# Kernel optimization log

Measured on AMD Instinct MI355X. Metric: run time of the kernel, lower is better.

Reference implementation:

```python
import jax, jax.numpy as jnp
import numpy as np

N = 50000
E = 800000
IN_C, HID_C, OUT_C = 512, 128, 64


def setup_inputs() -> dict:
    key = jax.random.key(0)
    k = jax.random.split(key, 8)
    x = jax.random.normal(k[0], (N, IN_C), dtype=jnp.float32)
    edge_index = jax.random.randint(k[1], (2, E), 0, N, dtype=jnp.int64)
    edge_weight = jax.random.uniform(k[2], (E,), dtype=jnp.float32)
    # GCNConv parameters (glorot-like init)
    W1 = jax.random.normal(k[3], (IN_C, HID_C), dtype=jnp.float32) * (1.0 / np.sqrt(IN_C))
    b1 = jnp.zeros((HID_C,), dtype=jnp.float32)
    W2 = jax.random.normal(k[4], (HID_C, OUT_C), dtype=jnp.float32) * (1.0 / np.sqrt(HID_C))
    b2 = jnp.zeros((OUT_C,), dtype=jnp.float32)
    return {"x": x, "edge_index": edge_index, "edge_weight": edge_weight,
            "W1": W1, "b1": b1, "W2": W2, "b2": b2}


def _add_self_loops(edge_index, edge_weight, num_nodes):
    loop = jnp.arange(num_nodes, dtype=edge_index.dtype)
    ei = jnp.concatenate([edge_index, jnp.stack([loop, loop])], axis=1)
    ew = jnp.concatenate([edge_weight, jnp.ones((num_nodes,), edge_weight.dtype)])
    return ei, ew


def _gcn_conv(x, row, col, norm, W, b, num_nodes):
    # linear transform first (PyG GCNConv), then normalized scatter-add aggregation
    xw = x @ W                                    # [N, F_out]
    msg = norm[:, None] * xw[row]                 # gather + scale, [E', F_out]
    out = jnp.zeros((num_nodes, xw.shape[1]), xw.dtype).at[col].add(msg)
    return out + b


def reference(x, edge_index, edge_weight, W1, b1, W2, b2):
    num_nodes = x.shape[0]
    ei, ew = _add_self_loops(edge_index, edge_weight, num_nodes)
    row, col = ei[0], ei[1]
    # symmetric normalization: D^{-1/2} A D^{-1/2} (deg over destination index)
    deg = jnp.zeros((num_nodes,), ew.dtype).at[col].add(ew)
    dinv = jnp.where(deg > 0, jax.lax.rsqrt(deg), 0.0)
    norm = dinv[row] * ew * dinv[col]
    h = _gcn_conv(x, row, col, norm, W1, b1, num_nodes)
    h = jax.nn.relu(h)
    # dropout p=0.5 is identity in eval mode
    return _gcn_conv(h, row, col, norm, W2, b2, num_nodes)
```

## Files before the change

### kernel.cpp

```cpp
#include <hip/hip_runtime.h>

#define NNODES 50000
#define NEDGES 800000
#define IN_C   512
#define HID_C  128
#define OUT_C  64
#define NBUCK  196
#define BCAP   5120
#define BREG   5376

typedef float  f32x4  __attribute__((ext_vector_type(4)));
typedef __bf16 bf16x8 __attribute__((ext_vector_type(8)));
typedef short  short8 __attribute__((ext_vector_type(8)));

#define GLDS(src, dst) \
  __builtin_amdgcn_global_load_lds( \
      (const __attribute__((address_space(1))) unsigned int*)(src), \
      (__attribute__((address_space(3))) unsigned int*)(dst), 16, 0, 0)

__device__ __forceinline__ float bf2f(unsigned short u) {
  unsigned int x = (unsigned int)u << 16;
  return __builtin_bit_cast(float, x);
}
__device__ __forceinline__ unsigned short f16bits(float f) {
  _Float16 h = (_Float16)f;
  return __builtin_bit_cast(unsigned short, h);
}
__device__ __forceinline__ float f16val(unsigned short u) {
  return (float)__builtin_bit_cast(_Float16, u);
}


__device__ __forceinline__ void wsplit_one(const float* __restrict__ W,
                                           unsigned short* __restrict__ Th,
                                           unsigned short* __restrict__ Tl,
                                           int K, int N, int id) {
  int k = id % K, n = id / K;
  float f = W[(size_t)k * N + n];
  __bf16 hb = (__bf16)f;
  __bf16 lb = (__bf16)(f - (float)hb);
  Th[id] = __builtin_bit_cast(unsigned short, hb);
  Tl[id] = __builtin_bit_cast(unsigned short, lb);
}

__global__ void __launch_bounds__(256) prep0_kernel(
    unsigned int* __restrict__ gclaim,
    const float* __restrict__ W1, unsigned short* __restrict__ W1th,
    unsigned short* __restrict__ W1tl,
    const float* __restrict__ W2, unsigned short* __restrict__ W2th,
    unsigned short* __restrict__ W2tl) {
  int id = blockIdx.x * blockDim.x + threadIdx.x;
  if (id < 256) { if (id < NBUCK) gclaim[id] = (unsigned int)id * BCAP; return; }
  int s = id - 256;
  if (s < IN_C * HID_C) wsplit_one(W1, W1th, W1tl, IN_C, HID_C, s);
  else if (s < IN_C * HID_C + HID_C * OUT_C)
    wsplit_one(W2, W2th, W2tl, HID_C, OUT_C, s - IN_C * HID_C);
}


__global__ void __launch_bounds__(1024) bin_scatter_kernel(
    const int* __restrict__ ei, const float* __restrict__ ew,
    unsigned int* __restrict__ gclaim, unsigned long long* __restrict__ binned, int nE) {
  __shared__ unsigned int h[NBUCK];
  __shared__ unsigned int cur[NBUCK];
  int t = threadIdx.x;
  if (t < NBUCK) h[t] = 0;
  __syncthreads();
  int base = blockIdx.x * 8192;
  int r[8]; unsigned int c[8]; unsigned short wb[8];
#pragma unroll
  for (int i = 0; i < 8; ++i) {
    int e = base + i * 1024 + t;
    if (e < nE) {
      r[i] = ei[e];
      c[i] = (unsigned int)ei[nE + e];
      wb[i] = f16bits(ew[e]);
      atomicAdd(&h[c[i] >> 8], 1u);
    } else {
      c[i] = 0xFFFFFFFFu;
    }
  }
  __syncthreads();
  if (t < NBUCK) cur[t] = h[t] ? atomicAdd(&gclaim[t], h[t]) : 0u;
  __syncthreads();
#pragma unroll
  for (int i = 0; i < 8; ++i) {
    if (c[i] != 0xFFFFFFFFu) {
      unsigned int pos = atomicAdd(&cur[c[i] >> 8], 1u);
      unsigned long long rec = (unsigned long long)((unsigned int)r[i] & 0xFFFFu)
                             | ((unsigned long long)(c[i] & 0xFFu) << 16)
                             | ((unsigned long long)wb[i] << 32);
      binned[pos] = rec;
    }
  }
}


__global__ void __launch_bounds__(256) bucket_deg_kernel(
    const unsigned long long* __restrict__ binned, const unsigned int* __restrict__ gclaim,
    float* __restrict__ dinv, int* __restrict__ offs, unsigned short* __restrict__ cnts) {
  int b = blockIdx.x, t = threadIdx.x;
  int base = b * BCAP;
  int cnt = (int)gclaim[b] - base;
  int nb = min(256, NNODES - b * 256);
  __shared__ unsigned int ec[256], wf[256];
  __shared__ int sc[256];
  ec[t] = 0; wf[t] = 0;
  __syncthreads();
  for (int i = t; i < cnt; i += 256) {
    unsigned long long rec = binned[base + i];
    int dlo = (int)((rec >> 16) & 255ULL);
    atomicAdd(&ec[dlo], 1u);
    float w = f16val((unsigned short)(rec >> 32));
    atomicAdd(&wf[dlo], (unsigned int)(w * 1048576.0f + 0.5f));
  }
  __syncthreads();
  int cn = (t < nb) ? (int)ec[t] + 1 : 0;
  sc[t] = cn;
  __syncthreads();
  for (int off = 1; off < 256; off <<= 1) {
    int u = (t >= off) ? sc[t - off] : 0;
    __syncthreads();
    sc[t] += u;
    __syncthreads();
  }
  if (t < nb) {
    float deg = (float)wf[t] * (1.0f / 1048576.0f) + 1.0f;
    int g = b * 256 + t;
    dinv[g] = rsqrtf(deg);
    offs[g] = b * BREG + sc[t] - cn;
    cnts[g] = (unsigned short)ec[t];
  }
}


__global__ void __launch_bounds__(256) bucket_fill_kernel(
    const unsigned long long* __restrict__ binned, const unsigned int* __restrict__ gclaim,
    const float* __restrict__ dinv, const int* __restrict__ offs,
    unsigned int* __restrict__ edges) {
  int b = blockIdx.x, t = threadIdx.x;
  int base = b * BCAP;
  int cnt = (int)gclaim[b] - base;
  int nb = min(256, NNODES - b * 256);
  int csrbase = b * BREG;
  __shared__ unsigned int image[BREG];
  __shared__ unsigned int cur[256];
  __shared__ float ldv[256];
  float di = 0.f;
  if (t < nb) {
    int g = b * 256 + t;
    di = dinv[g];
    int loc = offs[g] - csrbase;
    cur[t] = (unsigned int)(loc + 1);
    image[loc] = (unsigned int)g | ((unsigned int)f16bits(di * di) << 16);
  }
  ldv[t] = di;
  __syncthreads();
  for (int i = t; i < cnt; i += 256) {
    unsigned long long rec = binned[base + i];
    int src = (int)(rec & 0xFFFFULL);
    int dlo = (int)((rec >> 16) & 255ULL);
    float w = f16val((unsigned short)(rec >> 32));
    float nm = dinv[src] * w * ldv[dlo];
    unsigned int pos = atomicAdd(&cur[dlo], 1u);
    image[pos] = (unsigned int)src | ((unsigned int)f16bits(nm) << 16);
  }
  __syncthreads();
  int total = cnt + nb;
  for (int j = t; j < total; j += 256) edges[csrbase + j] = image[j];
}

template <int K, int N, int WR, int WC>
__global__ void __launch_bounds__(WR * WC * 64, 4) gemm_mfma_kernel(
    const float* __restrict__ X, const unsigned short* __restrict__ Bth,
    const unsigned short* __restrict__ Btl, unsigned short* __restrict__ Y, int M) {
  constexpr int NW = WR * WC;
  constexpr int BM = WR * 32;
  constexpr int NI = K / 32;
  constexpr int ASLOTS = (BM / 8) / NW;
  constexpr int BSLOTS = (N / 8) / NW;

  __shared__ float          As[2][BM * 32];
  __shared__ unsigned short Bs[2][2][N * 32];

  int tid = threadIdx.x;
  int lane = tid & 63, wid = tid >> 6;
  int wr = wid / WC, wc = wid % WC;
  int row0blk = blockIdx.x * BM;
  int row0 = row0blk + wr * 32;
  int rlo = lane & 15;
  int khi = lane >> 4;

  f32x4 acc[2][4] = {};

  auto stage = [&](int t, int buf) {
    int kb = t * 32;
#pragma unroll
    for (int i = 0; i < ASLOTS; ++i) {
      int slot = wid * ASLOTS + i;
      int rt = slot * 8 + (lane >> 3);
      int gr = row0blk + rt; gr = gr < M ? gr : M - 1;
      int gs = (lane & 7) ^ (lane >> 3);
      GLDS(X + (size_t)gr * K + kb + gs * 4, &As[buf][slot * 256]);
    }
#pragma unroll
    for (int i = 0; i < BSLOTS; ++i) {
      int slot = wid * BSLOTS + i;
      int half = slot / (N / 16);
      int idx = slot % (N / 16);
      const unsigned short* Wt = half ? Btl : Bth;
      int c = idx * 16 + (lane >> 2);
      int gs = (lane & 3) ^ (lane >> 4);
      GLDS(Wt + (size_t)c * K + kb + gs * 8, &Bs[buf][half][idx * 512]);
    }
  };

  stage(0, 0);
  __syncthreads();

#pragma unroll 1
  for (int t = 0; t < NI; ++t) {
    int buf = t & 1;
    if (t + 1 < NI) stage(t + 1, buf ^ 1);

    bf16x8 ah[2], al[2];
#pragma unroll
    for (int m = 0; m < 2; ++m) {
      int rt = wr * 32 + m * 16 + rlo;
      int p0 = (khi * 2) ^ (rlo & 7), p1 = (khi * 2 + 1) ^ (rlo & 7);
      f32x4 v0 = *reinterpret_cast<const f32x4*>(&As[buf][rt * 32 + p0 * 4]);
      f32x4 v1 = *reinterpret_cast<const f32x4*>(&As[buf][rt * 32 + p1 * 4]);
      float f[8] = {v0.x, v0.y, v0.z, v0.w, v1.x, v1.y, v1.z, v1.w};
#pragma unroll
      for (int i = 0; i < 8; ++i) {
        __bf16 hv = (__bf16)f[i];
        ah[m][i] = hv;
        al[m][i] = (__bf16)(f[i] - (float)hv);
      }
    }
    short8 bh[4], bl[4];
#pragma unroll
    for (int n = 0; n < 4; ++n) {
      int c = wc * 64 + n * 16 + rlo;
      int pos = khi ^ (rlo >> 2);
      bh[n] = *reinterpret_cast<const short8*>(&Bs[buf][0][c * 32 + pos * 8]);
      bl[n] = *reinterpret_cast<const short8*>(&Bs[buf][1][c * 32 + pos * 8]);
    }
#pragma unroll
    for (int m = 0; m < 2; ++m)
#pragma unroll
      for (int n = 0; n < 4; ++n)
        acc[m][n] = __builtin_amdgcn_mfma_f32_16x16x32_bf16(
            ah[m], __builtin_bit_cast(bf16x8, bh[n]), acc[m][n], 0, 0, 0);
#pragma unroll
    for (int m = 0; m < 2; ++m)
#pragma unroll
      for (int n = 0; n < 4; ++n)
        acc[m][n] = __builtin_amdgcn_mfma_f32_16x16x32_bf16(
            al[m], __builtin_bit_cast(bf16x8, bh[n]), acc[m][n], 0, 0, 0);
#pragma unroll
    for (int m = 0; m < 2; ++m)
#pragma unroll
      for (int n = 0; n < 4; ++n)
        acc[m][n] = __builtin_amdgcn_mfma_f32_16x16x32_bf16(
            ah[m], __builtin_bit_cast(bf16x8, bl[n]), acc[m][n], 0, 0, 0);
    __syncthreads();
  }

#pragma unroll
  for (int m = 0; m < 2; ++m)
#pragma unroll
    for (int j = 0; j < 4; ++j) {
      int row = row0 + m * 16 + khi * 4 + j;
      if (row < M) {
#pragma unroll
        for (int n = 0; n < 4; ++n) {
          __bf16 q = (__bf16)acc[m][n][j];
          Y[(size_t)row * N + wc * 64 + n * 16 + rlo] = __builtin_bit_cast(unsigned short, q);
        }
      }
    }
}

template <int K, int N, int WR, int WC>
__global__ void __launch_bounds__(WR * WC * 64, 4) gemm_bf16a_kernel(
    const unsigned short* __restrict__ X, const unsigned short* __restrict__ Bth,
    const unsigned short* __restrict__ Btl, unsigned short* __restrict__ Y, int M) {
  constexpr int NW = WR * WC;
  constexpr int BM = WR * 32;
  constexpr int NI = K / 32;
  constexpr int ASLOTS = (BM / 16) / NW;
  constexpr int BSLOTS = (N / 8) / NW;

  __shared__ unsigned short As[2][BM * 32];
  __shared__ unsigned short Bs[2][2][N * 32];

  int tid = threadIdx.x;
  int lane = tid & 63, wid = tid >> 6;
  int wr = wid / WC, wc = wid % WC;
  int row0blk = blockIdx.x * BM;
  int row0 = row0blk + wr * 32;
  int rlo = lane & 15;
  int khi = lane >> 4;

  f32x4 acc[2][4] = {};

  auto stage = [&](int t, int buf) {
    int kb = t * 32;
#pragma unroll
    for (int i = 0; i < ASLOTS; ++i) {
      int slot = wid * ASLOTS + i;
      int rt = slot * 16 + (lane >> 2);
      int gr = row0blk + rt; gr = gr < M ? gr : M - 1;
      int gs = (lane & 3) ^ ((lane >> 3) & 3);
      GLDS(X + (size_t)gr * K + kb + gs * 8, &As[buf][slot * 512]);
    }
#pragma unroll
    for (int i = 0; i < BSLOTS; ++i) {
      int slot = wid * BSLOTS + i;
      int half = slot / (N / 16);
      int idx = slot % (N / 16);
      const unsigned short* Wt = half ? Btl : Bth;
      int c = idx * 16 + (lane >> 2);
      int gs = (lane & 3) ^ (lane >> 4);
      GLDS(Wt + (size_t)c * K + kb + gs * 8, &Bs[buf][half][idx * 512]);
    }
  };

  stage(0, 0);
  __syncthreads();

#pragma unroll 1
  for (int t = 0; t < NI; ++t) {
    int buf = t & 1;
    if (t + 1 < NI) stage(t + 1, buf ^ 1);

    short8 ah[2];
#pragma unroll
    for (int m = 0; m < 2; ++m) {
      int rt = wr * 32 + m * 16 + rlo;
      int g = khi ^ ((rt >> 1) & 3);
      ah[m] = *reinterpret_cast<const short8*>(&As[buf][rt * 32 + g * 8]);
    }
    short8 bh[4], bl[4];
#pragma unroll
    for (int n = 0; n < 4; ++n) {
      int c = wc * 64 + n * 16 + rlo;
      int pos = khi ^ (rlo >> 2);
      bh[n] = *reinterpret_cast<const short8*>(&Bs[buf][0][c * 32 + pos * 8]);
      bl[n] = *reinterpret_cast<const short8*>(&Bs[buf][1][c * 32 + pos * 8]);
    }
#pragma unroll
    for (int m = 0; m < 2; ++m)
#pragma unroll
      for (int n = 0; n < 4; ++n)
        acc[m][n] = __builtin_amdgcn_mfma_f32_16x16x32_bf16(
            __builtin_bit_cast(bf16x8, ah[m]), __builtin_bit_cast(bf16x8, bh[n]),
            acc[m][n], 0, 0, 0);
#pragma unroll
    for (int m = 0; m < 2; ++m)
#pragma unroll
      for (int n = 0; n < 4; ++n)
        acc[m][n] = __builtin_amdgcn_mfma_f32_16x16x32_bf16(
            __builtin_bit_cast(bf16x8, ah[m]), __builtin_bit_cast(bf16x8, bl[n]),
            acc[m][n], 0, 0, 0);
    __syncthreads();
  }

#pragma unroll
  for (int m = 0; m < 2; ++m)
#pragma unroll
    for (int j = 0; j < 4; ++j) {
      int row = row0 + m * 16 + khi * 4 + j;
      if (row < M) {
#pragma unroll
        for (int n = 0; n < 4; ++n) {
          __bf16 q = (__bf16)acc[m][n][j];
          Y[(size_t)row * N + wc * 64 + n * 16 + rlo] = __builtin_bit_cast(unsigned short, q);
        }
      }
    }
}

template <int FSLICE, int FSTRIDE, bool RELU, bool OUTBF>
__global__ void __launch_bounds__(256) agg_kernel(const unsigned short* __restrict__ feat,
                                                  const int* __restrict__ offs,
                                                  const unsigned short* __restrict__ cnts,
                                                  const unsigned int* __restrict__ edges,
                                                  const float* __restrict__ bias,
                                                  void* __restrict__ outv, int foff, int n) {
  constexpr int LPN = FSLICE / 8;
  constexpr int NPW = 64 / LPN;
  constexpr int NPB = 4 * NPW;
  int wid = threadIdx.x >> 6;
  int lane = threadIdx.x & 63;
  int node = blockIdx.x * NPB + wid * NPW + lane / LPN;
  int lf = (lane % LPN) * 8;
  if (node >= n) return;
  int e0 = offs[node];
  int e1 = e0 + 1 + (int)cnts[node];
  const unsigned short* fp = feat + foff + lf;

  float acc[8];
#pragma unroll
  for (int j = 0; j < 8; ++j) acc[j] = bias[foff + lf + j];

  auto fmaEdge = [&](unsigned int q) {
    float w = f16val((unsigned short)(q >> 16));
    int row = (int)(q & 0xFFFFu);
    short8 v = *reinterpret_cast<const short8*>(fp + (size_t)row * FSTRIDE);
#pragma unroll
    for (int j = 0; j < 8; ++j)
      acc[j] = fmaf(w, bf2f((unsigned short)v[j]), acc[j]);
  };

  int e = e0;
  for (; e + 4 <= e1; e += 4) {
    unsigned int q0 = edges[e], q1 = edges[e + 1], q2 = edges[e + 2], q3 = edges[e + 3];
    fmaEdge(q0); fmaEdge(q1); fmaEdge(q2); fmaEdge(q3);
  }
  for (; e < e1; ++e) fmaEdge(edges[e]);

  if (RELU) {
#pragma unroll
    for (int j = 0; j < 8; ++j) acc[j] = fmaxf(acc[j], 0.f);
  }
  if constexpr (OUTBF) {
    short8 o;
#pragma unroll
    for (int j = 0; j < 8; ++j) {
      __bf16 q = (__bf16)acc[j];
      o[j] = (short)__builtin_bit_cast(unsigned short, q);
    }
    *reinterpret_cast<short8*>((unsigned short*)outv + (size_t)node * FSTRIDE + foff + lf) = o;
  } else {
    float* out = (float*)outv;
    float4 o0 = make_float4(acc[0], acc[1], acc[2], acc[3]);
    float4 o1 = make_float4(acc[4], acc[5], acc[6], acc[7]);
    *reinterpret_cast<float4*>(&out[(size_t)node * FSTRIDE + foff + lf]) = o0;
    *reinterpret_cast<float4*>(&out[(size_t)node * FSTRIDE + foff + lf + 4]) = o1;
  }
}


extern "C" void kernel_launch(void* const* d_in, const int* in_sizes, int n_in,
                              void* d_out, int out_size, void* d_ws, size_t ws_size,
                              hipStream_t stream) {
  const float* x  = (const float*)d_in[0];
  const int*   ei = (const int*)d_in[1];
  const float* ew = (const float*)d_in[2];
  const float* W1 = (const float*)d_in[3];
  const float* b1 = (const float*)d_in[4];
  const float* W2 = (const float*)d_in[5];
  const float* b2 = (const float*)d_in[6];
  float* out = (float*)d_out;

  const int N = NNODES, E = NEDGES;

  char* p = (char*)d_ws;
  auto alloc = [&](size_t bytes) { char* r = p; p += (bytes + 255) & ~(size_t)255; return r; };
  unsigned int* gclaim = (unsigned int*)alloc(256 * 4);
  float* dinv   = (float*)alloc((size_t)N * 4);
  int*   offs   = (int*)  alloc((size_t)N * 4);
  unsigned short* cnts = (unsigned short*)alloc((size_t)N * 2);
  unsigned long long* binned = (unsigned long long*)alloc((size_t)NBUCK * BCAP * 8);
  unsigned int* edges  = (unsigned int*)alloc((size_t)NBUCK * BREG * 4);
  unsigned short* xw = (unsigned short*)alloc((size_t)N * HID_C * 2);
  unsigned short* h  = (unsigned short*)alloc((size_t)N * HID_C * 2);
  unsigned short* W1th = (unsigned short*)alloc((size_t)IN_C * HID_C * 2);
  unsigned short* W1tl = (unsigned short*)alloc((size_t)IN_C * HID_C * 2);
  unsigned short* W2th = (unsigned short*)alloc((size_t)HID_C * OUT_C * 2);
  unsigned short* W2tl = (unsigned short*)alloc((size_t)HID_C * OUT_C * 2);

  const int PREP0 = 256 + IN_C * HID_C + HID_C * OUT_C;
  prep0_kernel<<<(PREP0 + 255) / 256, 256, 0, stream>>>(
      gclaim, W1, W1th, W1tl, W2, W2th, W2tl);

  const int NBLKE = (E + 8191) / 8192;
  bin_scatter_kernel<<<NBLKE, 1024, 0, stream>>>(ei, ew, gclaim, binned, E);

  gemm_mfma_kernel<IN_C, HID_C, 4, 2><<<(N + 127) / 128, 512, 0, stream>>>(x, W1th, W1tl, xw, N);

  bucket_deg_kernel<<<NBUCK, 256, 0, stream>>>(binned, gclaim, dinv, offs, cnts);
  bucket_fill_kernel<<<NBUCK, 256, 0, stream>>>(binned, gclaim, dinv, offs, edges);

  agg_kernel<64, HID_C, true, true><<<(N + 31) / 32, 256, 0, stream>>>(
      xw, offs, cnts, edges, b1, h, 0, N);
  agg_kernel<64, HID_C, true, true><<<(N + 31) / 32, 256, 0, stream>>>(
      xw, offs, cnts, edges, b1, h, 64, N);

  gemm_bf16a_kernel<HID_C, OUT_C, 8, 1><<<(N + 255) / 256, 512, 0, stream>>>(h, W2th, W2tl, xw, N);
  agg_kernel<64, OUT_C, false, false><<<(N + 31) / 32, 256, 0, stream>>>(
      xw, offs, cnts, edges, b2, out, 0, N);
}
```

Baseline: 117.4 us.

## Fuse layer-1 GEMM with edge binning and merge split aggregation passes

```diff
diff --git a/kernel.cpp b/kernel.cpp
--- a/kernel.cpp
+++ b/kernel.cpp
@@ -57,20 +57,138 @@
     wsplit_one(W2, W2th, W2tl, HID_C, OUT_C, s - IN_C * HID_C);
 }
 
-
-__global__ void __launch_bounds__(1024) bin_scatter_kernel(
-    const int* __restrict__ ei, const float* __restrict__ ew,
+template <int K, int N, int WR, int WC>
+__device__ __forceinline__ void gemm_body(const float* __restrict__ X,
+                                          const unsigned short* __restrict__ Bth,
+                                          const unsigned short* __restrict__ Btl,
+                                          unsigned short* __restrict__ Y, int M, int bid) {
+  constexpr int NW = WR * WC;
+  constexpr int BM = WR * 32;
+  constexpr int NI = K / 32;
+  constexpr int ASLOTS = (BM / 8) / NW;
+  constexpr int BSLOTS = (N / 8) / NW;
+
+  __shared__ float          As[2][BM * 32];
+  __shared__ unsigned short Bs[2][2][N * 32];
+
+  int tid = threadIdx.x;
+  int lane = tid & 63, wid = tid >> 6;
+  int wr = wid / WC, wc = wid % WC;
+  int row0blk = bid * BM;
+  int row0 = row0blk + wr * 32;
+  int rlo = lane & 15;
+  int khi = lane >> 4;
+
+  f32x4 acc[2][4] = {};
+
+  auto stage = [&](int t, int buf) {
+    int kb = t * 32;
+#pragma unroll
+    for (int i = 0; i < ASLOTS; ++i) {
+      int slot = wid * ASLOTS + i;
+      int rt = slot * 8 + (lane >> 3);
+      int gr = row0blk + rt; gr = gr < M ? gr : M - 1;
+      int gs = (lane & 7) ^ (lane >> 3);
+      GLDS(X + (size_t)gr * K + kb + gs * 4, &As[buf][slot * 256]);
+    }
+#pragma unroll
+    for (int i = 0; i < BSLOTS; ++i) {
+      int slot = wid * BSLOTS + i;
+      int half = slot / (N / 16);
+      int idx = slot % (N / 16);
+      const unsigned short* Wt = half ? Btl : Bth;
+      int c = idx * 16 + (lane >> 2);
+      int gs = (lane & 3) ^ (lane >> 4);
+      GLDS(Wt + (size_t)c * K + kb + gs * 8, &Bs[buf][half][idx * 512]);
+    }
+  };
+
+  stage(0, 0);
+  __syncthreads();
+
+#pragma unroll 1
+  for (int t = 0; t < NI; ++t) {
+    int buf = t & 1;
+    if (t + 1 < NI) stage(t + 1, buf ^ 1);
+
+    bf16x8 ah[2], al[2];
+#pragma unroll
+    for (int m = 0; m < 2; ++m) {
+      int rt = wr * 32 + m * 16 + rlo;
+      int p0 = (khi * 2) ^ (rlo & 7), p1 = (khi * 2 + 1) ^ (rlo & 7);
+      f32x4 v0 = *reinterpret_cast<const f32x4*>(&As[buf][rt * 32 + p0 * 4]);
+      f32x4 v1 = *reinterpret_cast<const f32x4*>(&As[buf][rt * 32 + p1 * 4]);
+      float f[8] = {v0.x, v0.y, v0.z, v0.w, v1.x, v1.y, v1.z, v1.w};
+#pragma unroll
+      for (int i = 0; i < 8; ++i) {
+        __bf16 hv = (__bf16)f[i];
+        ah[m][i] = hv;
+        al[m][i] = (__bf16)(f[i] - (float)hv);
+      }
+    }
+    short8 bh[4], bl[4];
+#pragma unroll
+    for (int n = 0; n < 4; ++n) {
+      int c = wc * 64 + n * 16 + rlo;
+      int pos = khi ^ (rlo >> 2);
+      bh[n] = *reinterpret_cast<const short8*>(&Bs[buf][0][c * 32 + pos * 8]);
+      bl[n] = *reinterpret_cast<const short8*>(&Bs[buf][1][c * 32 + pos * 8]);
+    }
+#pragma unroll
+    for (int m = 0; m < 2; ++m)
+#pragma unroll
+      for (int n = 0; n < 4; ++n)
+        acc[m][n] = __builtin_amdgcn_mfma_f32_16x16x32_bf16(
+            ah[m], __builtin_bit_cast(bf16x8, bh[n]), acc[m][n], 0, 0, 0);
+#pragma unroll
+    for (int m = 0; m < 2; ++m)
+#pragma unroll
+      for (int n = 0; n < 4; ++n)
+        acc[m][n] = __builtin_amdgcn_mfma_f32_16x16x32_bf16(
+            al[m], __builtin_bit_cast(bf16x8, bh[n]), acc[m][n], 0, 0, 0);
+#pragma unroll
+    for (int m = 0; m < 2; ++m)
+#pragma unroll
+      for (int n = 0; n < 4; ++n)
+        acc[m][n] = __builtin_amdgcn_mfma_f32_16x16x32_bf16(
+            ah[m], __builtin_bit_cast(bf16x8, bl[n]), acc[m][n], 0, 0, 0);
+    __syncthreads();
+  }
+
+#pragma unroll
+  for (int m = 0; m < 2; ++m)
+#pragma unroll
+    for (int j = 0; j < 4; ++j) {
+      int row = row0 + m * 16 + khi * 4 + j;
+      if (row < M) {
+#pragma unroll
+        for (int n = 0; n < 4; ++n) {
+          __bf16 q = (__bf16)acc[m][n][j];
+          Y[(size_t)row * N + wc * 64 + n * 16 + rlo] = __builtin_bit_cast(unsigned short, q);
+        }
+      }
+    }
+}
+
+__global__ void __launch_bounds__(512, 4) fused_gemm1_scatter_kernel(
+    const float* __restrict__ X, const unsigned short* __restrict__ Bth,
+    const unsigned short* __restrict__ Btl, unsigned short* __restrict__ Y, int M,
+    int ngemm, const int* __restrict__ ei, const float* __restrict__ ew,
     unsigned int* __restrict__ gclaim, unsigned long long* __restrict__ binned, int nE) {
+  if ((int)blockIdx.x < ngemm) {
+    gemm_body<IN_C, HID_C, 4, 2>(X, Bth, Btl, Y, M, blockIdx.x);
+    return;
+  }
   __shared__ unsigned int h[NBUCK];
   __shared__ unsigned int cur[NBUCK];
   int t = threadIdx.x;
   if (t < NBUCK) h[t] = 0;
   __syncthreads();
-  int base = blockIdx.x * 8192;
+  int base = ((int)blockIdx.x - ngemm) * 4096;
   int r[8]; unsigned int c[8]; unsigned short wb[8];
 #pragma unroll
   for (int i = 0; i < 8; ++i) {
-    int e = base + i * 1024 + t;
+    int e = base + i * 512 + t;
     if (e < nE) {
       r[i] = ei[e];
       c[i] = (unsigned int)ei[nE + e];
@@ -171,118 +289,6 @@
 }
 
 template <int K, int N, int WR, int WC>
-__global__ void __launch_bounds__(WR * WC * 64, 4) gemm_mfma_kernel(
-    const float* __restrict__ X, const unsigned short* __restrict__ Bth,
-    const unsigned short* __restrict__ Btl, unsigned short* __restrict__ Y, int M) {
-  constexpr int NW = WR * WC;
-  constexpr int BM = WR * 32;
-  constexpr int NI = K / 32;
-  constexpr int ASLOTS = (BM / 8) / NW;
-  constexpr int BSLOTS = (N / 8) / NW;
-
-  __shared__ float          As[2][BM * 32];
-  __shared__ unsigned short Bs[2][2][N * 32];
-
-  int tid = threadIdx.x;
-  int lane = tid & 63, wid = tid >> 6;
-  int wr = wid / WC, wc = wid % WC;
-  int row0blk = blockIdx.x * BM;
-  int row0 = row0blk + wr * 32;
-  int rlo = lane & 15;
-  int khi = lane >> 4;
-
-  f32x4 acc[2][4] = {};
-
-  auto stage = [&](int t, int buf) {
-    int kb = t * 32;
-#pragma unroll
-    for (int i = 0; i < ASLOTS; ++i) {
-      int slot = wid * ASLOTS + i;
-      int rt = slot * 8 + (lane >> 3);
-      int gr = row0blk + rt; gr = gr < M ? gr : M - 1;
-      int gs = (lane & 7) ^ (lane >> 3);
-      GLDS(X + (size_t)gr * K + kb + gs * 4, &As[buf][slot * 256]);
-    }
-#pragma unroll
-    for (int i = 0; i < BSLOTS; ++i) {
-      int slot = wid * BSLOTS + i;
-      int half = slot / (N / 16);
-      int idx = slot % (N / 16);
-      const unsigned short* Wt = half ? Btl : Bth;
-      int c = idx * 16 + (lane >> 2);
-      int gs = (lane & 3) ^ (lane >> 4);
-      GLDS(Wt + (size_t)c * K + kb + gs * 8, &Bs[buf][half][idx * 512]);
-    }
-  };
-
-  stage(0, 0);
-  __syncthreads();
-
-#pragma unroll 1
-  for (int t = 0; t < NI; ++t) {
-    int buf = t & 1;
-    if (t + 1 < NI) stage(t + 1, buf ^ 1);
-
-    bf16x8 ah[2], al[2];
-#pragma unroll
-    for (int m = 0; m < 2; ++m) {
-      int rt = wr * 32 + m * 16 + rlo;
-      int p0 = (khi * 2) ^ (rlo & 7), p1 = (khi * 2 + 1) ^ (rlo & 7);
-      f32x4 v0 = *reinterpret_cast<const f32x4*>(&As[buf][rt * 32 + p0 * 4]);
-      f32x4 v1 = *reinterpret_cast<const f32x4*>(&As[buf][rt * 32 + p1 * 4]);
-      float f[8] = {v0.x, v0.y, v0.z, v0.w, v1.x, v1.y, v1.z, v1.w};
-#pragma unroll
-      for (int i = 0; i < 8; ++i) {
-        __bf16 hv = (__bf16)f[i];
-        ah[m][i] = hv;
-        al[m][i] = (__bf16)(f[i] - (float)hv);
-      }
-    }
-    short8 bh[4], bl[4];
-#pragma unroll
-    for (int n = 0; n < 4; ++n) {
-      int c = wc * 64 + n * 16 + rlo;
-      int pos = khi ^ (rlo >> 2);
-      bh[n] = *reinterpret_cast<const short8*>(&Bs[buf][0][c * 32 + pos * 8]);
-      bl[n] = *reinterpret_cast<const short8*>(&Bs[buf][1][c * 32 + pos * 8]);
-    }
-#pragma unroll
-    for (int m = 0; m < 2; ++m)
-#pragma unroll
-      for (int n = 0; n < 4; ++n)
-        acc[m][n] = __builtin_amdgcn_mfma_f32_16x16x32_bf16(
-            ah[m], __builtin_bit_cast(bf16x8, bh[n]), acc[m][n], 0, 0, 0);
-#pragma unroll
-    for (int m = 0; m < 2; ++m)
-#pragma unroll
-      for (int n = 0; n < 4; ++n)
-        acc[m][n] = __builtin_amdgcn_mfma_f32_16x16x32_bf16(
-            al[m], __builtin_bit_cast(bf16x8, bh[n]), acc[m][n], 0, 0, 0);
-#pragma unroll
-    for (int m = 0; m < 2; ++m)
-#pragma unroll
-      for (int n = 0; n < 4; ++n)
-        acc[m][n] = __builtin_amdgcn_mfma_f32_16x16x32_bf16(
-            ah[m], __builtin_bit_cast(bf16x8, bl[n]), acc[m][n], 0, 0, 0);
-    __syncthreads();
-  }
-
-#pragma unroll
-  for (int m = 0; m < 2; ++m)
-#pragma unroll
-    for (int j = 0; j < 4; ++j) {
-      int row = row0 + m * 16 + khi * 4 + j;
-      if (row < M) {
-#pragma unroll
-        for (int n = 0; n < 4; ++n) {
-          __bf16 q = (__bf16)acc[m][n][j];
-          Y[(size_t)row * N + wc * 64 + n * 16 + rlo] = __builtin_bit_cast(unsigned short, q);
-        }
-      }
-    }
-}
-
-template <int K, int N, int WR, int WC>
 __global__ void __launch_bounds__(WR * WC * 64, 4) gemm_bf16a_kernel(
     const unsigned short* __restrict__ X, const unsigned short* __restrict__ Bth,
     const unsigned short* __restrict__ Btl, unsigned short* __restrict__ Y, int M) {
@@ -476,20 +482,18 @@
   prep0_kernel<<<(PREP0 + 255) / 256, 256, 0, stream>>>(
       gclaim, W1, W1th, W1tl, W2, W2th, W2tl);
 
-  const int NBLKE = (E + 8191) / 8192;
-  bin_scatter_kernel<<<NBLKE, 1024, 0, stream>>>(ei, ew, gclaim, binned, E);
-
-  gemm_mfma_kernel<IN_C, HID_C, 4, 2><<<(N + 127) / 128, 512, 0, stream>>>(x, W1th, W1tl, xw, N);
+  const int NGEMM = (N + 127) / 128;
+  const int NSCAT = (E + 4095) / 4096;
+  fused_gemm1_scatter_kernel<<<NGEMM + NSCAT, 512, 0, stream>>>(
+      x, W1th, W1tl, xw, N, NGEMM, ei, ew, gclaim, binned, E);
 
   bucket_deg_kernel<<<NBUCK, 256, 0, stream>>>(binned, gclaim, dinv, offs, cnts);
   bucket_fill_kernel<<<NBUCK, 256, 0, stream>>>(binned, gclaim, dinv, offs, edges);
 
-  agg_kernel<64, HID_C, true, true><<<(N + 31) / 32, 256, 0, stream>>>(
+  agg_kernel<HID_C, HID_C, true, true><<<(N + 15) / 16, 256, 0, stream>>>(
       xw, offs, cnts, edges, b1, h, 0, N);
-  agg_kernel<64, HID_C, true, true><<<(N + 31) / 32, 256, 0, stream>>>(
-      xw, offs, cnts, edges, b1, h, 64, N);
 
   gemm_bf16a_kernel<HID_C, OUT_C, 8, 1><<<(N + 255) / 256, 512, 0, stream>>>(h, W2th, W2tl, xw, N);
-  agg_kernel<64, OUT_C, false, false><<<(N + 31) / 32, 256, 0, stream>>>(
+  agg_kernel<OUT_C, OUT_C, false, false><<<(N + 31) / 32, 256, 0, stream>>>(
       xw, offs, cnts, edges, b2, out, 0, N);
 }
```

Measured after the change: 107.3 us. 1.09x faster.
